# Optimization experiments

Hardware: AMD Instinct MI355X
Metric: run time of the kernel (lower is better)

The kernel has to match this reference:

```python
import jax, jax.numpy as jnp
import numpy as np

D_MODEL = 1024
NUM_HEADS = 16
THETA = 10000.0
B, S = 4, 2048


def setup_inputs() -> dict:
    key = jax.random.key(0)
    ks = jax.random.split(key, 5)
    scale = 1.0 / np.sqrt(D_MODEL)  # keep logits in a sane range
    return {
        "q_proj_weight": jax.random.normal(ks[0], (D_MODEL, D_MODEL), jnp.float32) * scale,
        "k_proj_weight": jax.random.normal(ks[1], (D_MODEL, D_MODEL), jnp.float32) * scale,
        "v_proj_weight": jax.random.normal(ks[2], (D_MODEL, D_MODEL), jnp.float32) * scale,
        "o_proj_weight": jax.random.normal(ks[3], (D_MODEL, D_MODEL), jnp.float32) * scale,
        "in_features": jax.random.normal(ks[4], (B, S, D_MODEL), jnp.float32),
        "token_positions": jnp.arange(S, dtype=jnp.int32),
    }


def _rope(x, cos, sin):
    # interleaved-pair RoPE: pairs are (x[..., 2i], x[..., 2i+1])
    xe = x[..., 0::2]
    xo = x[..., 1::2]
    re = xe * cos - xo * sin
    ro = xe * sin + xo * cos
    return jnp.stack([re, ro], axis=-1).reshape(x.shape)


def reference(q_proj_weight, k_proj_weight, v_proj_weight, o_proj_weight,
              in_features, token_positions):
    Bv, Sv, _ = in_features.shape
    dk = D_MODEL // NUM_HEADS
    half = dk // 2

    q = in_features @ q_proj_weight.T
    k = in_features @ k_proj_weight.T
    v = in_features @ v_proj_weight.T
    # (B, S, D) -> (B, H, S, dk)
    q = q.reshape(Bv, Sv, NUM_HEADS, dk).transpose(0, 2, 1, 3)
    k = k.reshape(Bv, Sv, NUM_HEADS, dk).transpose(0, 2, 1, 3)
    v = v.reshape(Bv, Sv, NUM_HEADS, dk).transpose(0, 2, 1, 3)

    inv_freq = 1.0 / (THETA ** (jnp.arange(half, dtype=jnp.float32) / half))
    freqs = token_positions.astype(jnp.float32)[:, None] * inv_freq[None, :]  # (S, half)
    cos, sin = jnp.cos(freqs), jnp.sin(freqs)  # broadcast over (B, H, S, half)
    q = _rope(q, cos, sin)
    k = _rope(k, cos, sin)

    scores = jnp.einsum('bhqd,bhkd->bhqk', q, k) / np.sqrt(dk).astype(np.float32)
    causal = jnp.tril(jnp.ones((Sv, Sv), dtype=bool))
    scores = jnp.where(causal, scores, -jnp.inf)
    weights = jax.nn.softmax(scores, axis=-1)
    out = jnp.einsum('bhqk,bhkd->bhqd', weights, v)
    out = out.transpose(0, 2, 1, 3).reshape(Bv, Sv, D_MODEL)
    return out @ o_proj_weight.T
```

## Files before the change

### kernel.cpp

```cpp
#include <hip/hip_runtime.h>
#include <stdint.h>
#include <math.h>

#define NH 16
#define DK 64
#define S_LEN 2048
#define BB 4
#define DM 1024
#define M_TOT (BB*S_LEN)
#define KVT 64
#define KPAD 72
#define QB 128

#define BM 256
#define BN 128
#define BK 64
#define NTK (DM/BK)
#define LDS_A_BUF (BM*BK)
#define LDS_B_BUF (BN*BK)

typedef __attribute__((ext_vector_type(8))) short short8;
typedef __attribute__((ext_vector_type(4))) float floatx4;

typedef const __attribute__((address_space(1))) void gas_t;
typedef __attribute__((address_space(3))) void las_t;

__device__ __forceinline__ void glds16(const void* g, void* l){
  __builtin_amdgcn_global_load_lds((gas_t*)g, (las_t*)l, 16, 0, 0);
}

#define VMCNT6() asm volatile("s_waitcnt vmcnt(6)" ::: "memory")
#define VMCNT0() asm volatile("s_waitcnt vmcnt(0)" ::: "memory")
#define LGKM0()  do{ asm volatile("s_waitcnt lgkmcnt(0)" ::: "memory"); __builtin_amdgcn_sched_barrier(0); }while(0)
#define BARRIER() asm volatile("s_barrier" ::: "memory")

__device__ __forceinline__ unsigned short f2bf(float f){
  unsigned int u = __float_as_uint(f);
  u += 0x7fffu + ((u >> 16) & 1u);
  return (unsigned short)(u >> 16);
}
__device__ __forceinline__ unsigned int pk_bf_trunc(float a, float b){
  return __builtin_amdgcn_perm(__float_as_uint(b), __float_as_uint(a), 0x07060302u);
}
__device__ __forceinline__ float fast_exp2(float x){
  return __builtin_amdgcn_exp2f(x);
}

__global__ void cast_kernel(const float* __restrict__ in, unsigned short* __restrict__ out, int n){
  int i = (blockIdx.x * blockDim.x + threadIdx.x) * 4;
  if (i < n){
    float4 v = *(const float4*)(in + i);
    ushort4 u;
    u.x = f2bf(v.x); u.y = f2bf(v.y); u.z = f2bf(v.z); u.w = f2bf(v.w);
    *(ushort4*)(out + i) = u;
  }
}

__device__ __forceinline__ void stage_part(const unsigned short* __restrict__ A,
                                           const unsigned short* __restrict__ Bm,
                                           int m0, int n0, int k0,
                                           unsigned short* As, unsigned short* Bs,
                                           int tid, int part)
{
  if (part == 0){
    #pragma unroll
    for (int j = 0; j < 2; j++){
      int c = j*512 + tid;
      int r = c >> 3;
      int sl = (c & 7) ^ (r & 7);
      glds16(&A[(size_t)(m0 + r)*DM + k0 + sl*8], (char*)As + (size_t)c*16);
    }
    int c = tid;
    int r = c >> 3;
    int sl = (c & 7) ^ (r & 7);
    glds16(&Bm[(size_t)(n0 + r)*DM + k0 + sl*8], (char*)Bs + (size_t)c*16);
  } else {
    #pragma unroll
    for (int j = 2; j < 4; j++){
      int c = j*512 + tid;
      int r = c >> 3;
      int sl = (c & 7) ^ (r & 7);
      glds16(&A[(size_t)(m0 + r)*DM + k0 + sl*8], (char*)As + (size_t)c*16);
    }
    int c = 512 + tid;
    int r = c >> 3;
    int sl = (c & 7) ^ (r & 7);
    glds16(&Bm[(size_t)(n0 + r)*DM + k0 + sl*8], (char*)Bs + (size_t)c*16);
  }
}

__device__ __forceinline__ void gemm_core(const unsigned short* __restrict__ A,
                                          const unsigned short* __restrict__ Bm,
                                          int m0, int n0, unsigned short* Ls,
                                          int tid, floatx4 (&acc)[4][4])
{
  unsigned short* AsB = Ls;
  unsigned short* BsB = Ls + 3*LDS_A_BUF;
  int wave = tid >> 6, lane = tid & 63;
  int l15 = lane & 15, quad = lane >> 4;
  int wm = (wave >> 1) * 64, wn = (wave & 1) * 64;
  int s0 = quad ^ (l15 & 7);

  stage_part(A, Bm, m0, n0, 0,  AsB,             BsB,             tid, 0);
  stage_part(A, Bm, m0, n0, 0,  AsB,             BsB,             tid, 1);
  stage_part(A, Bm, m0, n0, BK, AsB + LDS_A_BUF, BsB + LDS_B_BUF, tid, 0);
  stage_part(A, Bm, m0, n0, BK, AsB + LDS_A_BUF, BsB + LDS_B_BUF, tid, 1);
  VMCNT6();
  BARRIER();

  #pragma unroll
  for (int t = 0; t < NTK; ++t){
    const int bufc = t % 3;
    const unsigned short* Ab = AsB + bufc*LDS_A_BUF;
    const unsigned short* Bb = BsB + bufc*LDS_B_BUF;
    const int bn = (t + 2) % 3;
    unsigned short* Asn = AsB + bn*LDS_A_BUF;
    unsigned short* Bsn = BsB + bn*LDS_B_BUF;
    const int kst = (t + 2) * BK;

    short8 a[2][2], b[4][2];
    #pragma unroll
    for (int mi = 0; mi < 2; mi++){
      const unsigned short* pr = Ab + (wm + mi*16 + l15)*BK;
      a[mi][0] = *(const short8*)(pr + s0*8);
      a[mi][1] = *(const short8*)(pr + (s0^4)*8);
    }
    #pragma unroll
    for (int ni = 0; ni < 4; ni++){
      const unsigned short* pr = Bb + (wn + ni*16 + l15)*BK;
      b[ni][0] = *(const short8*)(pr + s0*8);
      b[ni][1] = *(const short8*)(pr + (s0^4)*8);
    }
    if (t + 2 < NTK) stage_part(A, Bm, m0, n0, kst, Asn, Bsn, tid, 0);
    BARRIER();
    LGKM0();
    __builtin_amdgcn_s_setprio(1);
    #pragma unroll
    for (int mi = 0; mi < 2; mi++)
      #pragma unroll
      for (int ni = 0; ni < 4; ni++){
        acc[mi][ni] = __builtin_amdgcn_mfma_f32_16x16x32_bf16(a[mi][0], b[ni][0], acc[mi][ni], 0, 0, 0);
        acc[mi][ni] = __builtin_amdgcn_mfma_f32_16x16x32_bf16(a[mi][1], b[ni][1], acc[mi][ni], 0, 0, 0);
      }
    __builtin_amdgcn_s_setprio(0);
    BARRIER();

    short8 a2[2][2];
    #pragma unroll
    for (int mi = 0; mi < 2; mi++){
      const unsigned short* pr = Ab + (wm + (2 + mi)*16 + l15)*BK;
      a2[mi][0] = *(const short8*)(pr + s0*8);
      a2[mi][1] = *(const short8*)(pr + (s0^4)*8);
    }
    if (t + 2 < NTK) stage_part(A, Bm, m0, n0, kst, Asn, Bsn, tid, 1);
    BARRIER();
    LGKM0();
    __builtin_amdgcn_s_setprio(1);
    #pragma unroll
    for (int mi = 0; mi < 2; mi++)
      #pragma unroll
      for (int ni = 0; ni < 4; ni++){
        acc[2+mi][ni] = __builtin_amdgcn_mfma_f32_16x16x32_bf16(a2[mi][0], b[ni][0], acc[2+mi][ni], 0, 0, 0);
        acc[2+mi][ni] = __builtin_amdgcn_mfma_f32_16x16x32_bf16(a2[mi][1], b[ni][1], acc[2+mi][ni], 0, 0, 0);
      }
    __builtin_amdgcn_s_setprio(0);

    if (t + 2 < NTK)      { VMCNT6(); BARRIER(); }
    else if (t + 1 < NTK) { VMCNT0(); BARRIER(); }
  }
}

__global__ __launch_bounds__(512, 2) void gemm_qkv(
    const unsigned short* __restrict__ Xb,
    const unsigned short* __restrict__ Wq,
    const unsigned short* __restrict__ Wk,
    const unsigned short* __restrict__ Wv,
    const int* __restrict__ pos,
    unsigned short* __restrict__ Qo,
    unsigned short* __restrict__ Ko,
    unsigned short* __restrict__ VTo)
{
  __shared__ __align__(16) unsigned short Ls[3*LDS_A_BUF + 3*LDS_B_BUF];
  int m0 = blockIdx.x * BM;
  int n0 = blockIdx.y * BN;
  int z  = blockIdx.z;
  const unsigned short* Bmat = (z == 0) ? Wq : ((z == 1) ? Wk : Wv);
  unsigned short* Out = (z == 0) ? Qo : ((z == 1) ? Ko : VTo);

  int tid = threadIdx.x;
  floatx4 acc[4][4] = {};
  gemm_core(Xb, Bmat, m0, n0, Ls, tid, acc);

  int wave = tid >> 6, lane = tid & 63;
  int l15 = lane & 15, quad = lane >> 4;
  int wm = (wave >> 1) * 64, wn = (wave & 1) * 64;

  if (z == 2){
    #pragma unroll
    for (int mi = 0; mi < 4; mi++){
      int row0 = m0 + wm + mi * 16 + quad * 4;
      int bb2 = row0 >> 11, sQ = row0 & (S_LEN - 1);
      #pragma unroll
      for (int ni = 0; ni < 4; ni++){
        int col = n0 + wn + ni * 16 + l15;
        int h = col >> 6, d = col & 63;
        ushort4 u;
        u.x = f2bf(acc[mi][ni][0]); u.y = f2bf(acc[mi][ni][1]);
        u.z = f2bf(acc[mi][ni][2]); u.w = f2bf(acc[mi][ni][3]);
        *(ushort4*)&Out[(((size_t)bb2 * NH + h) * DK + d) * S_LEN + sQ] = u;
      }
    }
  } else {
    const float SC = (z == 0) ? 0.180336879f : 1.0f;
    #pragma unroll
    for (int mi = 0; mi < 4; mi++){
      #pragma unroll
      for (int ni = 0; ni < 4; ni++){
        int col = n0 + wn + ni * 16 + l15;
        int h = col >> 6, d = col & 63;
        int fi = d >> 1, odd = d & 1;
        float invfrev = fast_exp2(-(float)fi * (13.2877123795494f / 32.0f)) * 0.15915494309f;
        #pragma unroll
        for (int r = 0; r < 4; r++){
          int row = m0 + wm + mi * 16 + quad * 4 + r;
          int bb2 = row >> 11, s = row & (S_LEN - 1);
          float p = (float)pos[s];
          float rev = p * invfrev;
          rev = rev - floorf(rev);
          float c  = __builtin_amdgcn_cosf(rev);
          float sn = __builtin_amdgcn_sinf(rev);
          float val = acc[mi][ni][r];
          float other = __shfl_xor(val, 1);
          float outv = odd ? (other * sn + val * c) : (val * c - other * sn);
          Out[(((size_t)bb2 * NH + h) * S_LEN + s) * DK + d] = f2bf(outv * SC);
        }
      }
    }
  }
}

__global__ __launch_bounds__(512, 2) void gemm_out(
    const unsigned short* __restrict__ Ab,
    const unsigned short* __restrict__ Wo,
    float* __restrict__ Out)
{
  __shared__ __align__(16) unsigned short Ls[3*LDS_A_BUF + 3*LDS_B_BUF];
  int m0 = blockIdx.x * BM;
  int n0 = blockIdx.y * BN;

  int tid = threadIdx.x;
  floatx4 acc[4][4] = {};
  gemm_core(Ab, Wo, m0, n0, Ls, tid, acc);

  int wave = tid >> 6, lane = tid & 63;
  int l15 = lane & 15, quad = lane >> 4;
  int wm = (wave >> 1) * 64, wn = (wave & 1) * 64;

  #pragma unroll
  for (int mi = 0; mi < 4; mi++){
    #pragma unroll
    for (int ni = 0; ni < 4; ni++){
      #pragma unroll
      for (int r = 0; r < 4; r++){
        int row = m0 + wm + mi * 16 + quad * 4 + r;
        int col = n0 + wn + ni * 16 + l15;
        Out[(size_t)row * DM + col] = acc[mi][ni][r];
      }
    }
  }
}

__global__ __launch_bounds__(256) void attn_kernel(
    const unsigned short* __restrict__ Qg,
    const unsigned short* __restrict__ Kg,
    const unsigned short* __restrict__ VTg,
    unsigned short* __restrict__ Ao)
{
  __shared__ __align__(16) unsigned short Ks[KVT * KPAD];
  __shared__ __align__(16) unsigned short Vs[DK * KPAD];
  __shared__ __align__(16) unsigned short Ps[4][32 * KPAD];

  int bh = blockIdx.x;
  int q0 = ((int)gridDim.y - 1 - (int)blockIdx.y) * QB;
  int tid = threadIdx.x, wave = tid >> 6, lane = tid & 63;
  int l15 = lane & 15, quad = lane >> 4;
  int qw = q0 + wave * 32;

  const unsigned short* Qb = Qg + (size_t)bh * S_LEN * DK;
  const unsigned short* Kb = Kg + (size_t)bh * S_LEN * DK;
  const unsigned short* Vb = VTg + (size_t)bh * DK * S_LEN;

  short8 aq[2][2];
  #pragma unroll
  for (int mi = 0; mi < 2; mi++){
    aq[mi][0] = *(const short8*)&Qb[(qw + mi * 16 + l15) * DK + quad * 8];
    aq[mi][1] = *(const short8*)&Qb[(qw + mi * 16 + l15) * DK + 32 + quad * 8];
  }

  floatx4 o[2][4] = {};
  float lsum[2][4] = {{0.f,0.f,0.f,0.f},{0.f,0.f,0.f,0.f}};

  int srow = tid >> 2;
  int scol = (tid & 3) * 16;
  int kpos = (srow & 3) * 16 + (srow >> 2);
  const unsigned short* Krow = Kb + (size_t)srow * DK + scol;
  const unsigned short* Vrow = Vb + (size_t)srow * S_LEN + scol;
  unsigned short* KsW = &Ks[kpos * KPAD + scol];
  unsigned short* VsW = &Vs[srow * KPAD + scol];

  int nt = q0 / KVT + 2;

  short8 kr0 = *(const short8*)(Krow);
  short8 kr1 = *(const short8*)(Krow + 8);
  short8 vr0 = *(const short8*)(Vrow);
  short8 vr1 = *(const short8*)(Vrow + 8);

  for (int kt = 0; kt < nt; kt++){
    int kv0 = kt * KVT;
    __syncthreads();
    *(short8*)(KsW)     = kr0;
    *(short8*)(KsW + 8) = kr1;
    *(short8*)(VsW)     = vr0;
    *(short8*)(VsW + 8) = vr1;
    if (kt + 1 < nt){
      int kvn = kv0 + KVT;
      kr0 = *(const short8*)(Krow + (size_t)kvn * DK);
      kr1 = *(const short8*)(Krow + (size_t)kvn * DK + 8);
      vr0 = *(const short8*)(Vrow + kvn);
      vr1 = *(const short8*)(Vrow + kvn + 8);
    }
    __syncthreads();

    if (kv0 <= qw + 31){
      floatx4 sc[2][4] = {};
      #pragma unroll
      for (int ni = 0; ni < 4; ni++){
        short8 bk0 = *(const short8*)&Ks[(ni * 16 + l15) * KPAD + quad * 8];
        short8 bk1 = *(const short8*)&Ks[(ni * 16 + l15) * KPAD + 32 + quad * 8];
        #pragma unroll
        for (int mi = 0; mi < 2; mi++){
          sc[mi][ni] = __builtin_amdgcn_mfma_f32_16x16x32_bf16(aq[mi][0], bk0, sc[mi][ni], 0, 0, 0);
          sc[mi][ni] = __builtin_amdgcn_mfma_f32_16x16x32_bf16(aq[mi][1], bk1, sc[mi][ni], 0, 0, 0);
        }
      }
      bool full = (kv0 + 63 <= qw);
      int kvb = kv0 + 4 * l15;
      #pragma unroll
      for (int mi = 0; mi < 2; mi++){
        #pragma unroll
        for (int r = 0; r < 4; r++){
          int qg = qw + mi * 16 + quad * 4 + r;
          float v0 = sc[mi][0][r], v1 = sc[mi][1][r], v2 = sc[mi][2][r], v3 = sc[mi][3][r];
          if (!full){
            v0 = (kvb     > qg) ? -INFINITY : v0;
            v1 = (kvb + 1 > qg) ? -INFINITY : v1;
            v2 = (kvb + 2 > qg) ? -INFINITY : v2;
            v3 = (kvb + 3 > qg) ? -INFINITY : v3;
          }
          float p0 = fast_exp2(v0);
          float p1 = fast_exp2(v1);
          float p2 = fast_exp2(v2);
          float p3 = fast_exp2(v3);
          lsum[mi][r] += (p0 + p1) + (p2 + p3);
          uint2 u;
          u.x = pk_bf_trunc(p0, p1);
          u.y = pk_bf_trunc(p2, p3);
          *(uint2*)&Ps[wave][(mi * 16 + quad * 4 + r) * KPAD + 4 * l15] = u;
        }
      }
      asm volatile("s_waitcnt lgkmcnt(0)" ::: "memory");
      short8 ap[2][2];
      #pragma unroll
      for (int mi = 0; mi < 2; mi++){
        ap[mi][0] = *(const short8*)&Ps[wave][(mi * 16 + l15) * KPAD + quad * 8];
        ap[mi][1] = *(const short8*)&Ps[wave][(mi * 16 + l15) * KPAD + 32 + quad * 8];
      }
      #pragma unroll
      for (int dt = 0; dt < 4; dt++){
        short8 bv0 = *(const short8*)&Vs[(dt * 16 + l15) * KPAD + quad * 8];
        short8 bv1 = *(const short8*)&Vs[(dt * 16 + l15) * KPAD + 32 + quad * 8];
        #pragma unroll
        for (int mi = 0; mi < 2; mi++){
          o[mi][dt] = __builtin_amdgcn_mfma_f32_16x16x32_bf16(ap[mi][0], bv0, o[mi][dt], 0, 0, 0);
          o[mi][dt] = __builtin_amdgcn_mfma_f32_16x16x32_bf16(ap[mi][1], bv1, o[mi][dt], 0, 0, 0);
        }
      }
    }
  }

  float linv[2][4];
  #pragma unroll
  for (int mi = 0; mi < 2; mi++){
    #pragma unroll
    for (int r = 0; r < 4; r++){
      float rs = lsum[mi][r];
      rs += __shfl_xor(rs, 1);
      rs += __shfl_xor(rs, 2);
      rs += __shfl_xor(rs, 4);
      rs += __shfl_xor(rs, 8);
      linv[mi][r] = 1.0f / rs;
    }
  }

  int bq = bh >> 4, hq = bh & 15;
  #pragma unroll
  for (int mi = 0; mi < 2; mi++){
    #pragma unroll
    for (int dt = 0; dt < 4; dt++){
      #pragma unroll
      for (int r = 0; r < 4; r++){
        float val = o[mi][dt][r] * linv[mi][r];
        int s = qw + mi * 16 + quad * 4 + r;
        int d = dt * 16 + l15;
        Ao[(((size_t)bq * S_LEN + s) * NH + hq) * DK + d] = f2bf(val);
      }
    }
  }
}

extern "C" void kernel_launch(void* const* d_in, const int* in_sizes, int n_in,
                              void* d_out, int out_size, void* d_ws, size_t ws_size,
                              hipStream_t stream) {
  (void)in_sizes; (void)n_in; (void)out_size; (void)ws_size;
  const float* Wq = (const float*)d_in[0];
  const float* Wk = (const float*)d_in[1];
  const float* Wv = (const float*)d_in[2];
  const float* Wo = (const float*)d_in[3];
  const float* X  = (const float*)d_in[4];
  const int* pos  = (const int*)d_in[5];
  float* out = (float*)d_out;

  char* ws = (char*)d_ws;
  const size_t MB = 1024 * 1024;
  unsigned short* Xb  = (unsigned short*)(ws);
  unsigned short* Wqb = (unsigned short*)(ws + 16 * MB);
  unsigned short* Wkb = (unsigned short*)(ws + 18 * MB);
  unsigned short* Wvb = (unsigned short*)(ws + 20 * MB);
  unsigned short* Wob = (unsigned short*)(ws + 22 * MB);
  unsigned short* Qb  = (unsigned short*)(ws + 24 * MB);
  unsigned short* Kb  = (unsigned short*)(ws + 40 * MB);
  unsigned short* Vb  = (unsigned short*)(ws + 56 * MB);
  unsigned short* Ab  = (unsigned short*)(ws + 72 * MB);

  cast_kernel<<<8192, 256, 0, stream>>>(X,  Xb,  M_TOT * DM);
  cast_kernel<<<1024, 256, 0, stream>>>(Wq, Wqb, DM * DM);
  cast_kernel<<<1024, 256, 0, stream>>>(Wk, Wkb, DM * DM);
  cast_kernel<<<1024, 256, 0, stream>>>(Wv, Wvb, DM * DM);
  cast_kernel<<<1024, 256, 0, stream>>>(Wo, Wob, DM * DM);

  gemm_qkv<<<dim3(M_TOT/BM, DM/BN, 3), 512, 0, stream>>>(Xb, Wqb, Wkb, Wvb, pos, Qb, Kb, Vb);
  attn_kernel<<<dim3(64, S_LEN / QB), 256, 0, stream>>>(Qb, Kb, Vb, Ab);
  gemm_out<<<dim3(M_TOT/BM, DM/BN), 512, 0, stream>>>(Ab, Wob, out);
}
```

Baseline: 247.5 us.

## Software-pipeline GEMM LDS fragment loads across k-steps and merge weight casts

After: 239.8 us. 3.1% less time.

```diff
diff --git a/kernel.cpp b/kernel.cpp
--- a/kernel.cpp
+++ b/kernel.cpp
@@ -29,10 +29,12 @@
   __builtin_amdgcn_global_load_lds((gas_t*)g, (las_t*)l, 16, 0, 0);
 }
 
+#define VMCNT3() asm volatile("s_waitcnt vmcnt(3)" ::: "memory")
 #define VMCNT6() asm volatile("s_waitcnt vmcnt(6)" ::: "memory")
 #define VMCNT0() asm volatile("s_waitcnt vmcnt(0)" ::: "memory")
 #define LGKM0()  do{ asm volatile("s_waitcnt lgkmcnt(0)" ::: "memory"); __builtin_amdgcn_sched_barrier(0); }while(0)
 #define BARRIER() asm volatile("s_barrier" ::: "memory")
+#define SCHEDB() __builtin_amdgcn_sched_barrier(0)
 
 __device__ __forceinline__ unsigned short f2bf(float f){
   unsigned int u = __float_as_uint(f);
@@ -54,6 +56,19 @@
     u.x = f2bf(v.x); u.y = f2bf(v.y); u.z = f2bf(v.z); u.w = f2bf(v.w);
     *(ushort4*)(out + i) = u;
   }
+}
+__global__ void cast4_kernel(const float* __restrict__ a, const float* __restrict__ b,
+                             const float* __restrict__ c, const float* __restrict__ d,
+                             unsigned short* __restrict__ oa, unsigned short* __restrict__ ob,
+                             unsigned short* __restrict__ oc, unsigned short* __restrict__ od){
+  int z = blockIdx.y;
+  const float* s = (z==0)?a:(z==1)?b:(z==2)?c:d;
+  unsigned short* o = (z==0)?oa:(z==1)?ob:(z==2)?oc:od;
+  int i = (blockIdx.x * blockDim.x + threadIdx.x) * 4;
+  float4 v = *(const float4*)(s + i);
+  ushort4 u;
+  u.x = f2bf(v.x); u.y = f2bf(v.y); u.z = f2bf(v.z); u.w = f2bf(v.w);
+  *(ushort4*)(o + i) = u;
 }
 
 __device__ __forceinline__ void stage_part(const unsigned short* __restrict__ A,
@@ -101,72 +116,86 @@
   int wm = (wave >> 1) * 64, wn = (wave & 1) * 64;
   int s0 = quad ^ (l15 & 7);
 
+  short8 a01[2][2], a23[2][2], b[2][4][2];
+
   stage_part(A, Bm, m0, n0, 0,  AsB,             BsB,             tid, 0);
   stage_part(A, Bm, m0, n0, 0,  AsB,             BsB,             tid, 1);
   stage_part(A, Bm, m0, n0, BK, AsB + LDS_A_BUF, BsB + LDS_B_BUF, tid, 0);
   stage_part(A, Bm, m0, n0, BK, AsB + LDS_A_BUF, BsB + LDS_B_BUF, tid, 1);
   VMCNT6();
   BARRIER();
+  #pragma unroll
+  for (int mi = 0; mi < 2; mi++){
+    const unsigned short* pr = AsB + (wm + mi*16 + l15)*BK;
+    a01[mi][0] = *(const short8*)(pr + s0*8);
+    a01[mi][1] = *(const short8*)(pr + (s0^4)*8);
+  }
+  #pragma unroll
+  for (int ni = 0; ni < 4; ni++){
+    const unsigned short* pr = BsB + (wn + ni*16 + l15)*BK;
+    b[0][ni][0] = *(const short8*)(pr + s0*8);
+    b[0][ni][1] = *(const short8*)(pr + (s0^4)*8);
+  }
 
   #pragma unroll
   for (int t = 0; t < NTK; ++t){
-    const int bufc = t % 3;
-    const unsigned short* Ab = AsB + bufc*LDS_A_BUF;
-    const unsigned short* Bb = BsB + bufc*LDS_B_BUF;
-    const int bn = (t + 2) % 3;
-    unsigned short* Asn = AsB + bn*LDS_A_BUF;
-    unsigned short* Bsn = BsB + bn*LDS_B_BUF;
+    const int par = t & 1, nxt = par ^ 1;
+    const unsigned short* Ab  = AsB + (t % 3)*LDS_A_BUF;
+    const unsigned short* Abn = AsB + ((t+1) % 3)*LDS_A_BUF;
+    const unsigned short* Bbn = BsB + ((t+1) % 3)*LDS_B_BUF;
+    unsigned short* Ast = AsB + ((t+2) % 3)*LDS_A_BUF;
+    unsigned short* Bst = BsB + ((t+2) % 3)*LDS_B_BUF;
     const int kst = (t + 2) * BK;
 
-    short8 a[2][2], b[4][2];
+    LGKM0();
     #pragma unroll
     for (int mi = 0; mi < 2; mi++){
-      const unsigned short* pr = Ab + (wm + mi*16 + l15)*BK;
-      a[mi][0] = *(const short8*)(pr + s0*8);
-      a[mi][1] = *(const short8*)(pr + (s0^4)*8);
-    }
-    #pragma unroll
-    for (int ni = 0; ni < 4; ni++){
-      const unsigned short* pr = Bb + (wn + ni*16 + l15)*BK;
-      b[ni][0] = *(const short8*)(pr + s0*8);
-      b[ni][1] = *(const short8*)(pr + (s0^4)*8);
-    }
-    if (t + 2 < NTK) stage_part(A, Bm, m0, n0, kst, Asn, Bsn, tid, 0);
+      const unsigned short* pr = Ab + (wm + (2+mi)*16 + l15)*BK;
+      a23[mi][0] = *(const short8*)(pr + s0*8);
+      a23[mi][1] = *(const short8*)(pr + (s0^4)*8);
+    }
+    if (t + 2 < NTK) stage_part(A, Bm, m0, n0, kst, Ast, Bst, tid, 0);
+    SCHEDB();
+    __builtin_amdgcn_s_setprio(1);
+    #pragma unroll
+    for (int mi = 0; mi < 2; mi++)
+      #pragma unroll
+      for (int ni = 0; ni < 4; ni++){
+        acc[mi][ni] = __builtin_amdgcn_mfma_f32_16x16x32_bf16(a01[mi][0], b[par][ni][0], acc[mi][ni], 0, 0, 0);
+        acc[mi][ni] = __builtin_amdgcn_mfma_f32_16x16x32_bf16(a01[mi][1], b[par][ni][1], acc[mi][ni], 0, 0, 0);
+      }
+    __builtin_amdgcn_s_setprio(0);
+    if (t + 2 < NTK)      { VMCNT3(); }
+    else if (t + 1 < NTK) { VMCNT0(); }
     BARRIER();
+
     LGKM0();
+    if (t + 1 < NTK){
+      #pragma unroll
+      for (int mi = 0; mi < 2; mi++){
+        const unsigned short* pr = Abn + (wm + mi*16 + l15)*BK;
+        a01[mi][0] = *(const short8*)(pr + s0*8);
+        a01[mi][1] = *(const short8*)(pr + (s0^4)*8);
+      }
+      #pragma unroll
+      for (int ni = 0; ni < 4; ni++){
+        const unsigned short* pr = Bbn + (wn + ni*16 + l15)*BK;
+        b[nxt][ni][0] = *(const short8*)(pr + s0*8);
+        b[nxt][ni][1] = *(const short8*)(pr + (s0^4)*8);
+      }
+    }
+    if (t + 2 < NTK) stage_part(A, Bm, m0, n0, kst, Ast, Bst, tid, 1);
+    SCHEDB();
     __builtin_amdgcn_s_setprio(1);
     #pragma unroll
     for (int mi = 0; mi < 2; mi++)
       #pragma unroll
       for (int ni = 0; ni < 4; ni++){
-        acc[mi][ni] = __builtin_amdgcn_mfma_f32_16x16x32_bf16(a[mi][0], b[ni][0], acc[mi][ni], 0, 0, 0);
-        acc[mi][ni] = __builtin_amdgcn_mfma_f32_16x16x32_bf16(a[mi][1], b[ni][1], acc[mi][ni], 0, 0, 0);
+        acc[2+mi][ni] = __builtin_amdgcn_mfma_f32_16x16x32_bf16(a23[mi][0], b[par][ni][0], acc[2+mi][ni], 0, 0, 0);
+        acc[2+mi][ni] = __builtin_amdgcn_mfma_f32_16x16x32_bf16(a23[mi][1], b[par][ni][1], acc[2+mi][ni], 0, 0, 0);
       }
     __builtin_amdgcn_s_setprio(0);
-    BARRIER();
-
-    short8 a2[2][2];
-    #pragma unroll
-    for (int mi = 0; mi < 2; mi++){
-      const unsigned short* pr = Ab + (wm + (2 + mi)*16 + l15)*BK;
-      a2[mi][0] = *(const short8*)(pr + s0*8);
-      a2[mi][1] = *(const short8*)(pr + (s0^4)*8);
-    }
-    if (t + 2 < NTK) stage_part(A, Bm, m0, n0, kst, Asn, Bsn, tid, 1);
-    BARRIER();
-    LGKM0();
-    __builtin_amdgcn_s_setprio(1);
-    #pragma unroll
-    for (int mi = 0; mi < 2; mi++)
-      #pragma unroll
-      for (int ni = 0; ni < 4; ni++){
-        acc[2+mi][ni] = __builtin_amdgcn_mfma_f32_16x16x32_bf16(a2[mi][0], b[ni][0], acc[2+mi][ni], 0, 0, 0);
-        acc[2+mi][ni] = __builtin_amdgcn_mfma_f32_16x16x32_bf16(a2[mi][1], b[ni][1], acc[2+mi][ni], 0, 0, 0);
-      }
-    __builtin_amdgcn_s_setprio(0);
-
-    if (t + 2 < NTK)      { VMCNT6(); BARRIER(); }
-    else if (t + 1 < NTK) { VMCNT0(); BARRIER(); }
+    if (t + 1 < NTK) BARRIER();
   }
 }
 
@@ -443,10 +472,7 @@
   unsigned short* Ab  = (unsigned short*)(ws + 72 * MB);
 
   cast_kernel<<<8192, 256, 0, stream>>>(X,  Xb,  M_TOT * DM);
-  cast_kernel<<<1024, 256, 0, stream>>>(Wq, Wqb, DM * DM);
-  cast_kernel<<<1024, 256, 0, stream>>>(Wk, Wkb, DM * DM);
-  cast_kernel<<<1024, 256, 0, stream>>>(Wv, Wvb, DM * DM);
-  cast_kernel<<<1024, 256, 0, stream>>>(Wo, Wob, DM * DM);
+  cast4_kernel<<<dim3(1024, 4), 256, 0, stream>>>(Wq, Wk, Wv, Wo, Wqb, Wkb, Wvb, Wob);
 
   gemm_qkv<<<dim3(M_TOT/BM, DM/BN, 3), 512, 0, stream>>>(Xb, Wqb, Wkb, Wvb, pos, Qb, Kb, Vb);
   attn_kernel<<<dim3(64, S_LEN / QB), 256, 0, stream>>>(Qb, Kb, Vb, Ab);
```
